# Kernel tuning notes

Hardware: AMD Instinct MI355X
Metric: run time of the kernel (lower is better)

## Reference

```python
import jax, jax.numpy as jnp
import numpy as np

K = 3  # sparsify_graph default k


def _lstm_dir(x, Wi, Wh, b, reverse):
    # x: [B, T, Hin]; Wi: [Hin, 4H]; Wh: [H, 4H]; b: [4H]
    B = x.shape[0]
    H = Wh.shape[0]
    xs = jnp.swapaxes(x, 0, 1)  # [T, B, Hin]
    if reverse:
        xs = xs[::-1]

    def step(carry, xt):
        h, c = carry
        g = xt @ Wi + h @ Wh + b
        i, f, gg, o = jnp.split(g, 4, axis=-1)  # torch gate order i,f,g,o
        c = jax.nn.sigmoid(f) * c + jax.nn.sigmoid(i) * jnp.tanh(gg)
        h = jax.nn.sigmoid(o) * jnp.tanh(c)
        return (h, c), h

    h0 = jnp.zeros((B, H), x.dtype)
    _, hs = jax.lax.scan(step, (h0, h0), xs)
    if reverse:
        hs = hs[::-1]
    return jnp.swapaxes(hs, 0, 1)  # [B, T, H]


def setup_inputs() -> dict:
    key = jax.random.key(0)
    ks = jax.random.split(key, 24)
    B, T, C, F = 16, 256, 64, 128
    GO, H = 32, 32  # gat_out, lstm hidden
    s = 0.1
    return {
        "x": jax.random.normal(ks[0], (B, T, C, F), jnp.float32),
        "spectral_w": jax.random.normal(ks[1], (C, F), jnp.float32),
        "gat_W": jax.random.normal(ks[2], (F, GO), jnp.float32) * s,
        "gat_a": jax.random.normal(ks[3], (2 * GO,), jnp.float32),
        "pool_w": jax.random.normal(ks[4], (GO, 1), jnp.float32) * s,
        "pool_b": jnp.zeros((1,), jnp.float32),
        "lstm_Wi_f": jax.random.normal(ks[5], (GO, 4 * H), jnp.float32) * s,
        "lstm_Wh_f": jax.random.normal(ks[6], (H, 4 * H), jnp.float32) * s,
        "lstm_b_f": jnp.zeros((4 * H,), jnp.float32),
        "lstm_Wi_r": jax.random.normal(ks[7], (GO, 4 * H), jnp.float32) * s,
        "lstm_Wh_r": jax.random.normal(ks[8], (H, 4 * H), jnp.float32) * s,
        "lstm_b_r": jnp.zeros((4 * H,), jnp.float32),
        "ta_W": jax.random.normal(ks[9], (2 * H, 2 * H), jnp.float32) * s,
        "ta_b": jnp.zeros((2 * H,), jnp.float32),
        "ta_v": jax.random.normal(ks[10], (2 * H,), jnp.float32) * s,
        "ln_g": jnp.ones((2 * H,), jnp.float32),
        "ln_b": jnp.zeros((2 * H,), jnp.float32),
        "fc1_w": jax.random.normal(ks[11], (2 * H, 32), jnp.float32) * s,
        "fc1_b": jnp.zeros((32,), jnp.float32),
        "fc2_w": jax.random.normal(ks[12], (32, 3), jnp.float32) * s,
        "fc2_b": jnp.zeros((3,), jnp.float32),
    }


def reference(x, spectral_w, gat_W, gat_a, pool_w, pool_b,
              lstm_Wi_f, lstm_Wh_f, lstm_b_f, lstm_Wi_r, lstm_Wh_r, lstm_b_r,
              ta_W, ta_b, ta_v, ln_g, ln_b, fc1_w, fc1_b, fc2_w, fc2_b):
    B, T, C, F = x.shape
    # SpectralWeighting: per-(channel,feature) softmaxed weights over feature dim
    x = x * jax.nn.softmax(spectral_w, axis=-1)  # [B,T,C,F]

    # compute_graph per sample: mean_t of cosine-similarity Gram over channels
    Hn = x / (jnp.linalg.norm(x, axis=-1, keepdims=True) + 1e-8)
    A = jnp.einsum('btcf,btdf->bcd', Hn, Hn) / T  # [B,C,C]

    # sparsify_graph: per-row top-(K+1), drop diagonal, symmetrize mask
    _, idx = jax.lax.top_k(A, K + 1)  # [B,C,K+1]
    topk_mask = jnp.sum(jax.nn.one_hot(idx, C, dtype=jnp.float32), axis=2) > 0  # [B,C,C]
    eye = jnp.eye(C, dtype=bool)
    topk_mask = topk_mask & ~eye
    topk_mask = topk_mask | jnp.swapaxes(topk_mask, 1, 2)
    A = jnp.where(topk_mask, A, 0.0)

    # GAT layer, vectorized over (B, T) with shared per-sample adjacency
    Wh = jnp.einsum('btcf,fo->btco', x, gat_W)  # [B,T,C,32]
    O = Wh.shape[-1]
    s1 = Wh @ gat_a[:O]  # [B,T,C]  a . Wh_i
    s2 = Wh @ gat_a[O:]  # [B,T,C]  a . Wh_j
    e = jax.nn.leaky_relu(s1[..., :, None] + s2[..., None, :], 0.2)  # [B,T,C,C]
    amask = (A > 0) | eye  # [B,C,C]
    e = jnp.where(amask[:, None], e, -1e9)
    alpha = jax.nn.softmax(e, axis=-1)  # dropout skipped (eval mode)
    gat = jax.nn.relu(jnp.einsum('btcd,btdo->btco', alpha, Wh))  # [B,T,C,32]

    # ChannelAttentionPooling: softmax over channel dim
    w = jax.nn.softmax(gat @ pool_w + pool_b, axis=2)  # [B,T,C,1]
    h = jnp.sum(gat * w, axis=2)  # [B,T,32]

    # BiLSTM
    hf = _lstm_dir(h, lstm_Wi_f, lstm_Wh_f, lstm_b_f, False)
    hr = _lstm_dir(h, lstm_Wi_r, lstm_Wh_r, lstm_b_r, True)
    h = jnp.concatenate([hf, hr], axis=-1)  # [B,T,64]

    # TemporalAttention (dropout skipped, eval mode)
    sc = (jnp.tanh(h @ ta_W + ta_b) @ ta_v) / 1.5  # [B,T]
    al = jax.nn.softmax(sc, axis=1)
    ctx = jnp.sum(h * al[..., None], axis=1)  # [B,64]

    # LayerNorm
    mu = jnp.mean(ctx, axis=-1, keepdims=True)
    var = jnp.var(ctx, axis=-1, keepdims=True)
    ctx = (ctx - mu) / jnp.sqrt(var + 1e-5) * ln_g + ln_b

    # Classifier head (dropout skipped, eval mode)
    return jax.nn.relu(ctx @ fc1_w + fc1_b) @ fc2_w + fc2_b  # [B,3]
```

## Files before the change

### kernel.cpp

```cpp
#include <hip/hip_runtime.h>
#include <hip/hip_bf16.h>

#define B_  16
#define T_  256
#define C_  64
#define F_  128
#define O_  32
#define H_  32
#define G4_ 128

typedef __attribute__((ext_vector_type(8))) short bfrag;
typedef __attribute__((ext_vector_type(4))) float f4acc;

__device__ __forceinline__ unsigned short f2bf(float v) {
    union { float f; unsigned u; } c; c.f = v;
    unsigned r = c.u + 0x7FFF + ((c.u >> 16) & 1);
    return (unsigned short)(r >> 16);
}
__device__ __forceinline__ float bf2f(unsigned short b) {
    union { float f; unsigned u; } c; c.u = ((unsigned)b) << 16; return c.f;
}
__device__ __forceinline__ float sigm_f(float x) {
    return __builtin_amdgcn_rcpf(1.f + __expf(-x));
}
__device__ __forceinline__ float tanh_f(float x) {
    float e = __expf(2.f * x);
    return 1.f - 2.f * __builtin_amdgcn_rcpf(e + 1.f);
}
__device__ __forceinline__ float readlane_f(float v, int l) {
    return __int_as_float(__builtin_amdgcn_readlane(__float_as_int(v), l));
}

__global__ __launch_bounds__(64) void k_sw(const float* __restrict__ w,
                                           float* __restrict__ sw) {
    int c = blockIdx.x, lane = threadIdx.x;
    const float* row = w + c * F_;
    float v0 = row[lane], v1 = row[lane + 64];
    float m = fmaxf(v0, v1);
#pragma unroll
    for (int s = 1; s < 64; s <<= 1) m = fmaxf(m, __shfl_xor(m, s));
    float e0 = __expf(v0 - m), e1 = __expf(v1 - m);
    float s = e0 + e1;
#pragma unroll
    for (int s_ = 1; s_ < 64; s_ <<= 1) s += __shfl_xor(s, s_);
    sw[c * F_ + lane] = e0 / s;
    sw[c * F_ + lane + 64] = e1 / s;
}

#define TCP 2
#define PSTR 136

#define MFMA16(a, b, c) __builtin_amdgcn_mfma_f32_16x16x32_bf16(a, b, c, 0, 0, 0)

__global__ __launch_bounds__(256) void k_phase1(
    const float* __restrict__ x, const float* __restrict__ sw,
    const float* __restrict__ gat_W, const float* __restrict__ gat_a,
    float* __restrict__ A, float* __restrict__ Wh,
    float* __restrict__ s1, float* __restrict__ s2) {
    const int b = blockIdx.x, tc = blockIdx.y, tid = threadIdx.x;
    const int wv = tid >> 6, lane = tid & 63;
    const int quad = lane >> 4, l16 = lane & 15;

    __shared__ unsigned short hhi[64 * PSTR];
    __shared__ unsigned short hlo[64 * PSTR];
    __shared__ float nrm[64];
    __shared__ float s1p[2][64], s2p[2][64];

    float4 swr[8];
    {
        const float4* sw4 = (const float4*)sw;
#pragma unroll
        for (int i = 0; i < 8; i++) swr[i] = sw4[tid + 256 * i];
    }

    const int rt0 = (wv >> 1) * 2;
    const int ct0 = (wv & 1) * 2;
    const int jW = wv & 1;

    bfrag wfh[4], wfl[4];
    {
        const int n = l16 + 16 * jW;
#pragma unroll
        for (int k = 0; k < 4; k++) {
            union { unsigned short u[8]; bfrag v; } Hu, Lu;
#pragma unroll
            for (int u = 0; u < 8; u++) {
                float v = gat_W[(32 * k + quad * 8 + u) * O_ + n];
                unsigned short hb = f2bf(v);
                Hu.u[u] = hb;
                Lu.u[u] = f2bf(v - bf2f(hb));
            }
            wfh[k] = Hu.v;
            wfl[k] = Lu.v;
        }
    }
    const float ga1 = gat_a[l16 + 16 * jW];
    const float ga2 = gat_a[O_ + l16 + 16 * jW];

    f4acc accA[2][2];
#pragma unroll
    for (int i = 0; i < 2; i++)
#pragma unroll
        for (int j = 0; j < 2; j++) accA[i][j] = (f4acc){0.f, 0.f, 0.f, 0.f};

    for (int tt = 0; tt < TCP; ++tt) {
        const int t = tc * TCP + tt;
        const float4* xg = (const float4*)(x + ((size_t)(b * T_ + t) << 13));
        float4 xr[8];
#pragma unroll
        for (int i = 0; i < 8; i++) xr[i] = xg[tid + 256 * i];

        float invn_[8];
#pragma unroll
        for (int i = 0; i < 8; i++) {
            float4 v = xr[i], s = swr[i];
            v.x *= s.x; v.y *= s.y; v.z *= s.z; v.w *= s.w;
            xr[i] = v;
            float ss = v.x * v.x + v.y * v.y + v.z * v.z + v.w * v.w;
#pragma unroll
            for (int d = 1; d < 32; d <<= 1) ss += __shfl_xor(ss, d);
            float nv = sqrtf(ss) + 1e-8f;
            invn_[i] = 1.0f / nv;
            if ((tid & 31) == 0) nrm[(tid >> 5) + 8 * i] = nv;
        }
#pragma unroll
        for (int i = 0; i < 8; i++) {
            int c = (tid >> 5) + 8 * i;
            float4 v = xr[i];
            float iv = invn_[i];
            float a0 = v.x * iv, a1 = v.y * iv, a2 = v.z * iv, a3 = v.w * iv;
            union { unsigned short u[4]; unsigned long long q; } Hq, Lq;
            unsigned short h0 = f2bf(a0), h1 = f2bf(a1), h2 = f2bf(a2), h3 = f2bf(a3);
            Hq.u[0] = h0; Hq.u[1] = h1; Hq.u[2] = h2; Hq.u[3] = h3;
            Lq.u[0] = f2bf(a0 - bf2f(h0));
            Lq.u[1] = f2bf(a1 - bf2f(h1));
            Lq.u[2] = f2bf(a2 - bf2f(h2));
            Lq.u[3] = f2bf(a3 - bf2f(h3));
            int off = c * PSTR + 4 * (tid & 31);
            *(unsigned long long*)&hhi[off] = Hq.q;
            *(unsigned long long*)&hlo[off] = Lq.q;
        }
        __syncthreads();

        f4acc accW0 = (f4acc){0.f, 0.f, 0.f, 0.f};
        f4acc accW1 = (f4acc){0.f, 0.f, 0.f, 0.f};
#pragma unroll
        for (int k = 0; k < 4; k++) {
            const int ko = 32 * k + 8 * quad;
            bfrag r0h = *(const bfrag*)&hhi[(rt0 * 16 + l16) * PSTR + ko];
            bfrag r0l = *(const bfrag*)&hlo[(rt0 * 16 + l16) * PSTR + ko];
            bfrag r1h = *(const bfrag*)&hhi[((rt0 + 1) * 16 + l16) * PSTR + ko];
            bfrag r1l = *(const bfrag*)&hlo[((rt0 + 1) * 16 + l16) * PSTR + ko];
            bfrag c0h = *(const bfrag*)&hhi[(ct0 * 16 + l16) * PSTR + ko];
            bfrag c0l = *(const bfrag*)&hlo[(ct0 * 16 + l16) * PSTR + ko];
            bfrag c1h = *(const bfrag*)&hhi[((ct0 + 1) * 16 + l16) * PSTR + ko];
            bfrag c1l = *(const bfrag*)&hlo[((ct0 + 1) * 16 + l16) * PSTR + ko];
            accA[0][0] = MFMA16(r0h, c0h, accA[0][0]);
            accA[0][0] = MFMA16(r0h, c0l, accA[0][0]);
            accA[0][0] = MFMA16(r0l, c0h, accA[0][0]);
            accA[0][1] = MFMA16(r0h, c1h, accA[0][1]);
            accA[0][1] = MFMA16(r0h, c1l, accA[0][1]);
            accA[0][1] = MFMA16(r0l, c1h, accA[0][1]);
            accA[1][0] = MFMA16(r1h, c0h, accA[1][0]);
            accA[1][0] = MFMA16(r1h, c0l, accA[1][0]);
            accA[1][0] = MFMA16(r1l, c0h, accA[1][0]);
            accA[1][1] = MFMA16(r1h, c1h, accA[1][1]);
            accA[1][1] = MFMA16(r1h, c1l, accA[1][1]);
            accA[1][1] = MFMA16(r1l, c1h, accA[1][1]);
            accW0 = MFMA16(r0h, wfh[k], accW0);
            accW0 = MFMA16(r0h, wfl[k], accW0);
            accW0 = MFMA16(r0l, wfh[k], accW0);
            accW1 = MFMA16(r1h, wfh[k], accW1);
            accW1 = MFMA16(r1h, wfl[k], accW1);
            accW1 = MFMA16(r1l, wfh[k], accW1);
        }
        float* whout = Wh + (size_t)(b * T_ + t) * (C_ * O_);
#pragma unroll
        for (int i2 = 0; i2 < 2; i2++) {
            f4acc aw = i2 ? accW1 : accW0;
#pragma unroll
            for (int r = 0; r < 4; r++) {
                int row = (rt0 + i2) * 16 + quad * 4 + r;
                float val = aw[r] * nrm[row];
                whout[row * O_ + l16 + 16 * jW] = val;
                float v1 = val * ga1, v2 = val * ga2;
#pragma unroll
                for (int d = 1; d < 16; d <<= 1) {
                    v1 += __shfl_xor(v1, d);
                    v2 += __shfl_xor(v2, d);
                }
                if (l16 == 0) { s1p[jW][row] = v1; s2p[jW][row] = v2; }
            }
        }
        __syncthreads();
        if (tid < 64) {
            s1[(b * T_ + t) * C_ + tid] = s1p[0][tid] + s1p[1][tid];
            s2[(b * T_ + t) * C_ + tid] = s2p[0][tid] + s2p[1][tid];
        }
    }
#pragma unroll
    for (int i2 = 0; i2 < 2; i2++)
#pragma unroll
        for (int j2 = 0; j2 < 2; j2++)
#pragma unroll
            for (int r = 0; r < 4; r++) {
                int row = (rt0 + i2) * 16 + quad * 4 + r;
                int col = (ct0 + j2) * 16 + l16;
                atomicAdd(&A[b * (C_ * C_) + row * C_ + col], accA[i2][j2][r]);
            }
}

__global__ __launch_bounds__(64) void k_topk(const float* __restrict__ A,
                                             unsigned long long* __restrict__ amask) {
    int b = blockIdx.x;
    int c = threadIdx.x;
    __shared__ unsigned long long tk[C_];
    const float* row = A + b * (C_ * C_) + c * C_;
    unsigned long long sel = 0ULL;
    for (int r = 0; r < 4; r++) {
        float best = -1e30f;
        int bi = 0;
        for (int d = 0; d < C_; d++) {
            if (sel & (1ULL << d)) continue;
            float v = row[d];
            if (v > best) { best = v; bi = d; }
        }
        sel |= (1ULL << bi);
    }
    unsigned long long t = sel & ~(1ULL << c);
    tk[c] = t;
    __syncthreads();
    unsigned long long sym = t;
    for (int d = 0; d < C_; d++)
        if ((tk[d] >> c) & 1ULL) sym |= (1ULL << d);
    unsigned long long m = (1ULL << c);
    unsigned long long s2 = sym;
    while (s2) {
        int d = __ffsll(s2) - 1;
        s2 &= s2 - 1;
        if (row[d] > 0.f) m |= (1ULL << d);
    }
    amask[b * C_ + c] = m;
}

__global__ __launch_bounds__(256) void k_gat(
    const float* __restrict__ Wh, const float* __restrict__ s1,
    const float* __restrict__ s2, const unsigned long long* __restrict__ amask,
    const float* __restrict__ pool_w, const float* __restrict__ pool_b,
    const float* __restrict__ Wi_f, const float* __restrict__ b_f,
    const float* __restrict__ Wi_r, const float* __restrict__ b_r,
    float* __restrict__ gx) {
    int tg = blockIdx.x;
    int wv = threadIdx.x >> 6, c = threadIdx.x & 63;
    int bt = tg * 4 + wv;
    int b = bt >> 8;
    __shared__ float buf[4][C_][33];
    __shared__ float s2s[4][C_];
    __shared__ float hp[4][H_];

    s2s[wv][c] = s2[bt * C_ + c];
    float s1c = s1[bt * C_ + c];
    unsigned long long m = amask[b * C_ + c];
    __syncthreads();

    float mx = -1e30f;
    unsigned long long mm = m;
    while (mm) {
        int d = __ffsll(mm) - 1; mm &= mm - 1;
        float v = s1c + s2s[wv][d];
        v = v > 0.f ? v : 0.2f * v;
        mx = fmaxf(mx, v);
    }
    float ssum = 0.f;
    mm = m;
    while (mm) {
        int d = __ffsll(mm) - 1; mm &= mm - 1;
        float v = s1c + s2s[wv][d];
        v = v > 0.f ? v : 0.2f * v;
        ssum += __expf(v - mx);
    }
    float inv = 1.0f / ssum;
    float g[O_];
#pragma unroll
    for (int i = 0; i < O_; i++) g[i] = 0.f;
    mm = m;
    while (mm) {
        int d = __ffsll(mm) - 1; mm &= mm - 1;
        float v = s1c + s2s[wv][d];
        v = v > 0.f ? v : 0.2f * v;
        float a = __expf(v - mx);
        const float4* wr = (const float4*)(Wh + (size_t)bt * (C_ * O_) + d * O_);
#pragma unroll
        for (int q = 0; q < 8; q++) {
            float4 w4 = wr[q];
            g[4 * q + 0] += a * w4.x;
            g[4 * q + 1] += a * w4.y;
            g[4 * q + 2] += a * w4.z;
            g[4 * q + 3] += a * w4.w;
        }
    }
    float lg = pool_b[0];
#pragma unroll
    for (int i = 0; i < O_; i++) {
        g[i] = fmaxf(g[i] * inv, 0.f);
        lg += g[i] * pool_w[i];
    }
    float wmx = lg;
#pragma unroll
    for (int s = 1; s < 64; s <<= 1) wmx = fmaxf(wmx, __shfl_xor(wmx, s));
    float we = __expf(lg - wmx);
    float wsum = we;
#pragma unroll
    for (int s = 1; s < 64; s <<= 1) wsum += __shfl_xor(wsum, s);
    float wcf = we / wsum;
#pragma unroll
    for (int i = 0; i < O_; i++) buf[wv][c][i] = g[i] * wcf;
    __syncthreads();
    {
        int wt = threadIdx.x >> 6, o = threadIdx.x & 31, hf = (threadIdx.x >> 5) & 1;
        float sacc = 0.f;
#pragma unroll 8
        for (int d = hf * 32; d < hf * 32 + 32; d++) sacc += buf[wt][d][o];
        sacc += __shfl_xor(sacc, 32);
        if (hf == 0) hp[wt][o] = sacc;
    }
    __syncthreads();
    {
        int dir = threadIdx.x >> 7, col = threadIdx.x & 127;
        const float* Wi = dir ? Wi_r : Wi_f;
        const float* bb = dir ? b_r : b_f;
        float bv = bb[col];
        float a0 = bv, a1 = bv, a2 = bv, a3 = bv;
#pragma unroll
        for (int k = 0; k < H_; k++) {
            float wvv = Wi[k * G4_ + col];
            a0 = fmaf(hp[0][k], wvv, a0);
            a1 = fmaf(hp[1][k], wvv, a1);
            a2 = fmaf(hp[2][k], wvv, a2);
            a3 = fmaf(hp[3][k], wvv, a3);
        }
        size_t base = (size_t)dir * 4096 + (size_t)tg * 4;
        gx[(base + 0) * G4_ + col] = a0;
        gx[(base + 1) * G4_ + col] = a1;
        gx[(base + 2) * G4_ + col] = a2;
        gx[(base + 3) * G4_ + col] = a3;
    }
}

#define WW(k) float2 ww##k = make_float2(Wd[(k) * G4_ + lane], Wd[(k) * G4_ + lane + 64]);
#define KST(k, Aq) { float hk = readlane_f(h, k); \
    Aq.x = fmaf(hk, ww##k.x, Aq.x); Aq.y = fmaf(hk, ww##k.y, Aq.y); }

#define LSTEP(P) { \
    float2 A0 = make_float2(P##x, P##y); \
    float2 A1 = make_float2(0.f, 0.f); \
    float2 A2 = make_float2(0.f, 0.f); \
    float2 A3 = make_float2(0.f, 0.f); \
    P##x = q[lane]; P##y = q[lane + 64]; q += qstride; \
    KST(0, A0)  KST(1, A1)  KST(2, A2)  KST(3, A3) \
    KST(4, A0)  KST(5, A1)  KST(6, A2)  KST(7, A3) \
    KST(8, A0)  KST(9, A1)  KST(10, A2) KST(11, A3) \
    KST(12, A0) KST(13, A1) KST(14, A2) KST(15, A3) \
    KST(16, A0) KST(17, A1) KST(18, A2) KST(19, A3) \
    KST(20, A0) KST(21, A1) KST(22, A2) KST(23, A3) \
    KST(24, A0) KST(25, A1) KST(26, A2) KST(27, A3) \
    KST(28, A0) KST(29, A1) KST(30, A2) KST(31, A3) \
    float g0 = (A0.x + A1.x) + (A2.x + A3.x); \
    float g1 = (A0.y + A1.y) + (A2.y + A3.y); \
    float sA = sigm_f(g0); \
    float u = sigm_f(half_sel * g1); \
    float sB = (lane < 32) ? fmaf(2.f, u, -1.f) : u; \
    float sf = __shfl(sA, (lane & 31) + 32); \
    float so = __shfl(sB, (lane & 31) + 32); \
    cst = fmaf(sf, cst, sA * sB); \
    float hn = so * tanh_f(cst); \
    h = hn; \
    if (lane < H_) *hc = hn; \
    hc += hstride; \
}

__global__ void __attribute__((amdgpu_flat_work_group_size(64, 64)))
__attribute__((amdgpu_waves_per_eu(1, 1))) k_lstm_seq(
    const float* __restrict__ gx,
    const float* __restrict__ Whf, const float* __restrict__ Whr,
    float* __restrict__ hcat) {
    int dir = blockIdx.x & 1, b = blockIdx.x >> 1;
    int lane = threadIdx.x;
    const float* Wd = dir ? Whr : Whf;
    WW(0) WW(1) WW(2) WW(3) WW(4) WW(5) WW(6) WW(7)
    WW(8) WW(9) WW(10) WW(11) WW(12) WW(13) WW(14) WW(15)
    WW(16) WW(17) WW(18) WW(19) WW(20) WW(21) WW(22) WW(23)
    WW(24) WW(25) WW(26) WW(27) WW(28) WW(29) WW(30) WW(31)

    const float* gxb = gx + ((size_t)dir * 4096 + b * T_) * G4_;
    const int qstride = dir ? -G4_ : G4_;
    const float* q = gxb + (dir ? (T_ - 1) * G4_ : 0);
    float* hc = hcat + ((size_t)(b * T_) + (dir ? T_ - 1 : 0)) * (2 * H_)
                + dir * H_ + lane;
    const int hstride = dir ? -(2 * H_) : (2 * H_);

    float h = 0.f, cst = 0.f;
    const float half_sel = (lane < 32) ? 2.f : 1.f;

    float p0x = q[lane], p0y = q[lane + 64]; q += qstride;
    float p1x = q[lane], p1y = q[lane + 64]; q += qstride;
    float p2x = q[lane], p2y = q[lane + 64]; q += qstride;
    float p3x = q[lane], p3y = q[lane + 64]; q += qstride;

    for (int s = 0; s < T_; s += 4) {
        LSTEP(p0)
        LSTEP(p1)
        LSTEP(p2)
        LSTEP(p3)
    }
}

__global__ __launch_bounds__(256) void k_final(
    const float* __restrict__ hcat,
    const float* __restrict__ taW, const float* __restrict__ tab,
    const float* __restrict__ tav,
    const float* __restrict__ lng, const float* __restrict__ lnb,
    const float* __restrict__ w1, const float* __restrict__ b1,
    const float* __restrict__ w2, const float* __restrict__ b2,
    float* __restrict__ out) {
    int b = blockIdx.x;
    int t = threadIdx.x;
    __shared__ float Wl[64 * 64];
    __shared__ float al[T_];
    __shared__ float wred[4];
    __shared__ float ctxp[4][64];
    __shared__ float ctx[64];
    __shared__ float a1[32];
    for (int i = t; i < 4096; i += 256) Wl[i] = taW[i];
    float4 hr[16];
    const float4* hb = (const float4*)(hcat + ((size_t)b * T_ + t) * 64);
#pragma unroll
    for (int i = 0; i < 16; i++) hr[i] = hb[i];
    __syncthreads();
    float sc = 0.f;
    for (int j = 0; j < 64; j++) {
        float s = tab[j];
#pragma unroll
        for (int k4 = 0; k4 < 16; k4++) {
            float4 h4 = hr[k4];
            const float* wcol = &Wl[(4 * k4) * 64 + j];
            s += h4.x * wcol[0] + h4.y * wcol[64] + h4.z * wcol[128] + h4.w * wcol[192];
        }
        sc += tanhf(s) * tav[j];
    }
    sc *= (1.0f / 1.5f);
    int wave = t >> 6, lane = t & 63;
    float m = sc;
#pragma unroll
    for (int s_ = 1; s_ < 64; s_ <<= 1) m = fmaxf(m, __shfl_xor(m, s_));
    if (lane == 0) wred[wave] = m;
    __syncthreads();
    m = fmaxf(fmaxf(wred[0], wred[1]), fmaxf(wred[2], wred[3]));
    float e = __expf(sc - m);
    float ssum = e;
#pragma unroll
    for (int s_ = 1; s_ < 64; s_ <<= 1) ssum += __shfl_xor(ssum, s_);
    __syncthreads();
    if (lane == 0) wred[wave] = ssum;
    __syncthreads();
    float S = wred[0] + wred[1] + wred[2] + wred[3];
    al[t] = e / S;
    __syncthreads();
    {
        int o = t & 63, part = t >> 6;
        float cacc = 0.f;
        for (int tt = part * 64; tt < part * 64 + 64; tt++)
            cacc += al[tt] * hcat[((size_t)b * T_ + tt) * 64 + o];
        ctxp[part][o] = cacc;
    }
    __syncthreads();
    if (t < 64) {
        float ctxo = ctxp[0][t] + ctxp[1][t] + ctxp[2][t] + ctxp[3][t];
        float sv = ctxo, sq = ctxo * ctxo;
#pragma unroll
        for (int s_ = 1; s_ < 64; s_ <<= 1) {
            sv += __shfl_xor(sv, s_);
            sq += __shfl_xor(sq, s_);
        }
        float mu = sv * (1.f / 64.f);
        float var = sq * (1.f / 64.f) - mu * mu;
        ctx[t] = (ctxo - mu) / sqrtf(var + 1e-5f) * lng[t] + lnb[t];
    }
    __syncthreads();
    if (t < 32) {
        float s = b1[t];
        for (int k = 0; k < 64; k++) s += ctx[k] * w1[k * 32 + t];
        a1[t] = fmaxf(s, 0.f);
    }
    __syncthreads();
    if (t < 3) {
        float s = b2[t];
        for (int k = 0; k < 32; k++) s += a1[k] * w2[k * 3 + t];
        out[b * 3 + t] = s;
    }
}

extern "C" void kernel_launch(void* const* d_in, const int* in_sizes, int n_in,
                              void* d_out, int out_size, void* d_ws, size_t ws_size,
                              hipStream_t stream) {
    const float* x          = (const float*)d_in[0];
    const float* spectral_w = (const float*)d_in[1];
    const float* gat_W      = (const float*)d_in[2];
    const float* gat_a      = (const float*)d_in[3];
    const float* pool_w     = (const float*)d_in[4];
    const float* pool_b     = (const float*)d_in[5];
    const float* lstm_Wi_f  = (const float*)d_in[6];
    const float* lstm_Wh_f  = (const float*)d_in[7];
    const float* lstm_b_f   = (const float*)d_in[8];
    const float* lstm_Wi_r  = (const float*)d_in[9];
    const float* lstm_Wh_r  = (const float*)d_in[10];
    const float* lstm_b_r   = (const float*)d_in[11];
    const float* ta_W       = (const float*)d_in[12];
    const float* ta_b       = (const float*)d_in[13];
    const float* ta_v       = (const float*)d_in[14];
    const float* ln_g       = (const float*)d_in[15];
    const float* ln_b       = (const float*)d_in[16];
    const float* fc1_w      = (const float*)d_in[17];
    const float* fc1_b      = (const float*)d_in[18];
    const float* fc2_w      = (const float*)d_in[19];
    const float* fc2_b      = (const float*)d_in[20];
    float* out = (float*)d_out;

    float* ws = (float*)d_ws;
    float* sw    = ws + 0;
    float* A     = ws + 8192;
    unsigned long long* amask = (unsigned long long*)(ws + 73728);
    float* Wh    = ws + 75776;
    float* s1    = ws + 8464384;
    float* s2    = ws + 8726528;
    float* gx    = ws + 9119744;
    float* hcat  = ws + 10168320;

    hipMemsetAsync(A, 0, (size_t)C_ * C_ * B_ * sizeof(float), stream);
    k_sw<<<C_, 64, 0, stream>>>(spectral_w, sw);
    k_phase1<<<dim3(B_, T_ / TCP), 256, 0, stream>>>(x, sw, gat_W, gat_a, A, Wh, s1, s2);
    k_topk<<<B_, 64, 0, stream>>>(A, amask);
    k_gat<<<B_ * T_ / 4, 256, 0, stream>>>(Wh, s1, s2, amask, pool_w, pool_b,
                                           lstm_Wi_f, lstm_b_f, lstm_Wi_r, lstm_b_r, gx);
    k_lstm_seq<<<2 * B_, 64, 0, stream>>>(gx, lstm_Wh_f, lstm_Wh_r, hcat);
    k_final<<<B_, 256, 0, stream>>>(hcat, ta_W, ta_b, ta_v, ln_g, ln_b,
                                    fc1_w, fc1_b, fc2_w, fc2_b, out);
}
```

Baseline: 461.1 us.

## Store LSTM input gates time-contiguous per column for vector prefetch

The input-projection kernel now writes gx in a [dir][b][col][t] layout, with reverse-direction timesteps stored pre-reversed and written as float4. The sequential LSTM kernel can then read eight steps at a time per lane with float4 loads, prefetching the next block while computing the current one. This replaces the per-step strided scalar loads with a deeper prefetch. In exchange, the projection kernel's stores are now strided across columns instead of coalesced.

```diff
diff --git a/kernel.cpp b/kernel.cpp
--- a/kernel.cpp
+++ b/kernel.cpp
@@ -339,11 +339,14 @@
             a2 = fmaf(hp[2][k], wvv, a2);
             a3 = fmaf(hp[3][k], wvv, a3);
         }
-        size_t base = (size_t)dir * 4096 + (size_t)tg * 4;
-        gx[(base + 0) * G4_ + col] = a0;
-        gx[(base + 1) * G4_ + col] = a1;
-        gx[(base + 2) * G4_ + col] = a2;
-        gx[(base + 3) * G4_ + col] = a3;
+        int b0 = (tg * 4) >> 8;
+        int t0 = (tg * 4) & 255;
+        float* cb = gx + ((size_t)(dir * B_ + b0) * G4_ + col) * T_;
+        if (dir == 0) {
+            *(float4*)(cb + t0) = make_float4(a0, a1, a2, a3);
+        } else {
+            *(float4*)(cb + (252 - t0)) = make_float4(a3, a2, a1, a0);
+        }
     }
 }
 
@@ -351,12 +354,11 @@
 #define KST(k, Aq) { float hk = readlane_f(h, k); \
     Aq.x = fmaf(hk, ww##k.x, Aq.x); Aq.y = fmaf(hk, ww##k.y, Aq.y); }
 
-#define LSTEP(P) { \
-    float2 A0 = make_float2(P##x, P##y); \
+#define STEP(G0, G1) { \
+    float2 A0 = make_float2(G0, G1); \
     float2 A1 = make_float2(0.f, 0.f); \
     float2 A2 = make_float2(0.f, 0.f); \
     float2 A3 = make_float2(0.f, 0.f); \
-    P##x = q[lane]; P##y = q[lane + 64]; q += qstride; \
     KST(0, A0)  KST(1, A1)  KST(2, A2)  KST(3, A3) \
     KST(4, A0)  KST(5, A1)  KST(6, A2)  KST(7, A3) \
     KST(8, A0)  KST(9, A1)  KST(10, A2) KST(11, A3) \
@@ -392,9 +394,8 @@
     WW(16) WW(17) WW(18) WW(19) WW(20) WW(21) WW(22) WW(23)
     WW(24) WW(25) WW(26) WW(27) WW(28) WW(29) WW(30) WW(31)
 
-    const float* gxb = gx + ((size_t)dir * 4096 + b * T_) * G4_;
-    const int qstride = dir ? -G4_ : G4_;
-    const float* q = gxb + (dir ? (T_ - 1) * G4_ : 0);
+    const float* p0 = gx + ((size_t)(dir * B_ + b) * G4_ + lane) * T_;
+    const float* p1 = p0 + (size_t)64 * T_;
     float* hc = hcat + ((size_t)(b * T_) + (dir ? T_ - 1 : 0)) * (2 * H_)
                 + dir * H_ + lane;
     const int hstride = dir ? -(2 * H_) : (2 * H_);
@@ -402,16 +403,28 @@
     float h = 0.f, cst = 0.f;
     const float half_sel = (lane < 32) ? 2.f : 1.f;
 
-    float p0x = q[lane], p0y = q[lane + 64]; q += qstride;
-    float p1x = q[lane], p1y = q[lane + 64]; q += qstride;
-    float p2x = q[lane], p2y = q[lane + 64]; q += qstride;
-    float p3x = q[lane], p3y = q[lane + 64]; q += qstride;
-
-    for (int s = 0; s < T_; s += 4) {
-        LSTEP(p0)
-        LSTEP(p1)
-        LSTEP(p2)
-        LSTEP(p3)
+    float4 c0a = *(const float4*)(p0 + 0);
+    float4 c0b = *(const float4*)(p0 + 4);
+    float4 c1a = *(const float4*)(p1 + 0);
+    float4 c1b = *(const float4*)(p1 + 4);
+
+    for (int bi = 0; bi < 32; bi++) {
+        int o = (8 * (bi + 1)) & 255;
+        float4 n0a = *(const float4*)(p0 + o);
+        float4 n0b = *(const float4*)(p0 + o + 4);
+        float4 n1a = *(const float4*)(p1 + o);
+        float4 n1b = *(const float4*)(p1 + o + 4);
+
+        STEP(c0a.x, c1a.x)
+        STEP(c0a.y, c1a.y)
+        STEP(c0a.z, c1a.z)
+        STEP(c0a.w, c1a.w)
+        STEP(c0b.x, c1b.x)
+        STEP(c0b.y, c1b.y)
+        STEP(c0b.z, c1b.z)
+        STEP(c0b.w, c1b.w)
+
+        c0a = n0a; c0b = n0b; c1a = n1a; c1b = n1b;
     }
 }
 
```

Result: no change. 454.5 us (-1.4%).
